# Optimization experiments

Hardware: AMD Instinct MI355X
Metric: run time of the kernel (lower is better)

The kernel has to match this reference:

```python
import jax, jax.numpy as jnp
import numpy as np

N_NODES = 100000
EPS = 1e-5


def gcn_conv(x, edge_index, W, b):
    # PyG GCNConv: add self loops, symmetric normalization, aggregate at target.
    n = x.shape[0]
    xw = x @ W                                  # [N, F_out]
    loop = jnp.arange(n)
    src = jnp.concatenate([edge_index[0], loop])
    dst = jnp.concatenate([edge_index[1], loop])
    deg = jax.ops.segment_sum(jnp.ones_like(dst, dtype=xw.dtype), dst, num_segments=n)
    dinv = jnp.where(deg > 0, jax.lax.rsqrt(deg), 0.0)
    norm = dinv[src] * dinv[dst]                # [E+N]
    out = jax.ops.segment_sum(norm[:, None] * xw[src], dst, num_segments=n)
    return out + b


def batch_norm(x, gamma, beta):
    # training-mode BatchNorm1d over node dim
    m = x.mean(axis=0)
    v = x.var(axis=0)
    return (x - m) * jax.lax.rsqrt(v + EPS) * gamma + beta


def setup_inputs() -> dict:
    key = jax.random.key(0)
    ks = jax.random.split(key, 16)
    dims = [(128, 256), (256, 128), (128, 64)]
    inp = {
        "x": jax.random.normal(ks[0], (N_NODES, 128), dtype=jnp.float32),
        "edge_index": jax.random.randint(ks[1], (2, 1600000), 0, N_NODES),
        "pos_edge_index": jax.random.randint(ks[2], (2, 200000), 0, N_NODES),
        "neg_edge_index": jax.random.randint(ks[3], (2, 200000), 0, N_NODES),
    }
    for i, (fi, fo) in enumerate(dims, start=1):
        inp[f"W{i}"] = jax.random.normal(ks[3 + i], (fi, fo), dtype=jnp.float32) / np.sqrt(fi)
        inp[f"b{i}"] = jnp.zeros((fo,), dtype=jnp.float32)
        inp[f"g{i}"] = jnp.ones((fo,), dtype=jnp.float32)
        inp[f"beta{i}"] = jnp.zeros((fo,), dtype=jnp.float32)
    return inp


def reference(x, edge_index, pos_edge_index, neg_edge_index,
              W1, b1, g1, beta1, W2, b2, g2, beta2, W3, b3, g3, beta3):
    # encode
    h = gcn_conv(x, edge_index, W1, b1)
    h = jax.nn.sigmoid(batch_norm(h, g1, beta1))
    h = gcn_conv(h, edge_index, W2, b2)
    h = jax.nn.sigmoid(batch_norm(h, g2, beta2))
    h = gcn_conv(h, edge_index, W3, b3)
    z = batch_norm(h, g3, beta3)                # [N, 64]
    # decode
    ei = jnp.concatenate([pos_edge_index, neg_edge_index], axis=-1)
    logits = jnp.sum(z[ei[0]] * z[ei[1]], axis=-1)
    return logits
```

## Files before the change

### kernel.cpp

```cpp
#include <hip/hip_runtime.h>
#include <hip/hip_bf16.h>
#include <stddef.h>


#define WAVE 64
#define BSHIFT 9
#define SCHUNK 4096

typedef __attribute__((ext_vector_type(8))) short short8;
typedef __attribute__((ext_vector_type(4))) float f32x4;

__device__ __forceinline__ float bl(uint g) { return __uint_as_float(g << 16); }
__device__ __forceinline__ float bh(uint g) { return __uint_as_float(g & 0xffff0000u); }
__device__ __forceinline__ ushort f2b(float f) {
    uint u = __float_as_uint(f);
    return (ushort)((u + 0x7fffu + ((u >> 16) & 1u)) >> 16);
}
__device__ __forceinline__ uint pack2(float lo, float hi) {
    return (uint)f2b(lo) | ((uint)f2b(hi) << 16);
}

__device__ __forceinline__ void gload16(const ushort* g, ushort* l) {
    __builtin_amdgcn_global_load_lds(
        (const __attribute__((address_space(1))) uint*)g,
        (__attribute__((address_space(3))) uint*)l, 16, 0, 0);
}

__global__ __launch_bounds__(256) void k_bhist(const int* __restrict__ dst, int* __restrict__ gh, int E) {
    __shared__ int lh[256];
    lh[threadIdx.x] = 0; __syncthreads();
    int i = blockIdx.x * 256 + threadIdx.x, stride = gridDim.x * 256;
    for (; i < E; i += stride) atomicAdd(&lh[dst[i] >> BSHIFT], 1);
    __syncthreads();
    int v = lh[threadIdx.x];
    if (v) atomicAdd(&gh[threadIdx.x], v);
}

__global__ void k_bscan(const int* __restrict__ gh, int* __restrict__ boff, int* __restrict__ bcur) {
    __shared__ int ls[256];
    int t = threadIdx.x;
    int v = gh[t];
    ls[t] = v; __syncthreads();
    for (int off = 1; off < 256; off <<= 1) {
        int x = (t >= off) ? ls[t - off] : 0;
        __syncthreads();
        ls[t] += x;
        __syncthreads();
    }
    int excl = ls[t] - v;
    boff[t] = excl; bcur[t] = excl;
    if (t == 255) boff[256] = ls[255];
}

__global__ __launch_bounds__(256) void k_bscatter(const int* __restrict__ src, const int* __restrict__ dst,
                                                  int* __restrict__ gcur, uint* __restrict__ pairs, int E) {
    __shared__ int lh[256];
    int t = threadIdx.x;
    int base = blockIdx.x * SCHUNK;
    lh[t] = 0; __syncthreads();
    int rs[16], rd[16];
    #pragma unroll
    for (int i = 0; i < 16; ++i) {
        int idx = base + i * 256 + t;
        if (idx < E) { rs[i] = src[idx]; rd[i] = dst[idx]; atomicAdd(&lh[rd[i] >> BSHIFT], 1); }
        else rd[i] = -1;
    }
    __syncthreads();
    int cnt_b = lh[t];
    int b0 = cnt_b ? atomicAdd(&gcur[t], cnt_b) : 0;
    lh[t] = b0;
    __syncthreads();
    #pragma unroll
    for (int i = 0; i < 16; ++i) {
        if (rd[i] >= 0) {
            int p = atomicAdd(&lh[rd[i] >> BSHIFT], 1);
            pairs[p] = ((uint)(rd[i] & 511) << 17) | (uint)rs[i];
        }
    }
}

__global__ __launch_bounds__(256) void k_bfine(const uint* __restrict__ pairs, const int* __restrict__ boff,
                                               int* __restrict__ rowptr, int* __restrict__ srcs,
                                               float* __restrict__ dinv, int N, int E) {
    __shared__ int lcnt[512];
    __shared__ int ls[256];
    int b = blockIdx.x, t = threadIdx.x;
    int d0 = b << BSHIFT;
    int e0 = boff[b], e1 = boff[b + 1];
    lcnt[t] = 0; lcnt[t + 256] = 0;
    __syncthreads();
    for (int e = e0 + t; e < e1; e += 256)
        atomicAdd(&lcnt[pairs[e] >> 17], 1);
    __syncthreads();
    int c0 = lcnt[2 * t], c1 = lcnt[2 * t + 1];
    ls[t] = c0 + c1;
    __syncthreads();
    for (int off = 1; off < 256; off <<= 1) {
        int x = (t >= off) ? ls[t - off] : 0;
        __syncthreads();
        ls[t] += x;
        __syncthreads();
    }
    int excl = ls[t] - (c0 + c1);
    int s0 = excl, s1 = excl + c0;
    int d = d0 + 2 * t;
    if (d < N)     { rowptr[d] = e0 + s0;     dinv[d] = rsqrtf((float)(c0 + 1)); }
    if (d + 1 < N) { rowptr[d + 1] = e0 + s1; dinv[d + 1] = rsqrtf((float)(c1 + 1)); }
    if (b == 0 && t == 0) rowptr[N] = E;
    lcnt[2 * t] = s0; lcnt[2 * t + 1] = s1;
    __syncthreads();
    for (int e = e0 + t; e < e1; e += 256) {
        uint p = pairs[e];
        int pos = atomicAdd(&lcnt[p >> 17], 1);
        srcs[e0 + pos] = (int)(p & 0x1FFFFu);
    }
}

__global__ void k_conv(const float* __restrict__ W1, const float* __restrict__ W2,
                       const float* __restrict__ W3, ushort* __restrict__ Wt1,
                       ushort* __restrict__ Wt2, ushort* __restrict__ Wt3,
                       const float* __restrict__ x, const float* __restrict__ dinv,
                       ushort* __restrict__ xs, size_t n4) {
    size_t i = (size_t)blockIdx.x * 256 + threadIdx.x;
    if (i < 73728) {
        const float* W; ushort* Wt; int K, Nn; size_t j;
        if (i < 32768)      { W = W1; Wt = Wt1; K = 128; Nn = 256; j = i; }
        else if (i < 65536) { W = W2; Wt = Wt2; K = 256; Nn = 128; j = i - 32768; }
        else                { W = W3; Wt = Wt3; K = 128; Nn = 64;  j = i - 65536; }
        int k = (int)(j / Nn), n = (int)(j % Nn);
        Wt[(size_t)n * K + k] = f2b(W[(size_t)k * Nn + n]);
        return;
    }
    size_t j = i - 73728;
    if (j >= n4) return;
    float d = dinv[j / 32];
    float4 v = reinterpret_cast<const float4*>(x)[j];
    uint2 o;
    o.x = pack2(d * v.x, d * v.y);
    o.y = pack2(d * v.z, d * v.w);
    reinterpret_cast<uint2*>(xs)[j] = o;
}

template<int F>
__global__ __launch_bounds__(256) void k_agg(const ushort* __restrict__ in, ushort* __restrict__ out,
                                             const int* __restrict__ rowptr, const int* __restrict__ srcs,
                                             const float* __restrict__ dinv, int N) {
    constexpr int L = (F * 2) / 16;
    int wv = threadIdx.x >> 6, lane = threadIdx.x & 63;
    int node = (blockIdx.x * 4 + wv) * (64 / L) + lane / L;
    int sl = lane % L;
    if (node >= N) return;
    const uint4* inq = reinterpret_cast<const uint4*>(in);
    float di = dinv[node];
    float acc[8];
    {
        uint4 v = inq[(size_t)node * L + sl];
        acc[0] = bl(v.x); acc[1] = bh(v.x);
        acc[2] = bl(v.y); acc[3] = bh(v.y);
        acc[4] = bl(v.z); acc[5] = bh(v.z);
        acc[6] = bl(v.w); acc[7] = bh(v.w);
    }
    int e = rowptr[node], e1 = rowptr[node + 1];
    for (; e + 7 < e1; e += 8) {
        int s[8];
        #pragma unroll
        for (int i = 0; i < 8; ++i) s[i] = srcs[e + i];
        uint4 v[8];
        #pragma unroll
        for (int i = 0; i < 8; ++i) v[i] = inq[(size_t)s[i] * L + sl];
        #pragma unroll
        for (int i = 0; i < 8; ++i) {
            acc[0] += bl(v[i].x); acc[1] += bh(v[i].x);
            acc[2] += bl(v[i].y); acc[3] += bh(v[i].y);
            acc[4] += bl(v[i].z); acc[5] += bh(v[i].z);
            acc[6] += bl(v[i].w); acc[7] += bh(v[i].w);
        }
    }
    for (; e + 3 < e1; e += 4) {
        int s[4];
        #pragma unroll
        for (int i = 0; i < 4; ++i) s[i] = srcs[e + i];
        uint4 v[4];
        #pragma unroll
        for (int i = 0; i < 4; ++i) v[i] = inq[(size_t)s[i] * L + sl];
        #pragma unroll
        for (int i = 0; i < 4; ++i) {
            acc[0] += bl(v[i].x); acc[1] += bh(v[i].x);
            acc[2] += bl(v[i].y); acc[3] += bh(v[i].y);
            acc[4] += bl(v[i].z); acc[5] += bh(v[i].z);
            acc[6] += bl(v[i].w); acc[7] += bh(v[i].w);
        }
    }
    for (; e < e1; ++e) {
        uint4 v0 = inq[(size_t)srcs[e] * L + sl];
        acc[0] += bl(v0.x); acc[1] += bh(v0.x);
        acc[2] += bl(v0.y); acc[3] += bh(v0.y);
        acc[4] += bl(v0.z); acc[5] += bh(v0.z);
        acc[6] += bl(v0.w); acc[7] += bh(v0.w);
    }
    uint4 o;
    o.x = pack2(acc[0] * di, acc[1] * di);
    o.y = pack2(acc[2] * di, acc[3] * di);
    o.z = pack2(acc[4] * di, acc[5] * di);
    o.w = pack2(acc[6] * di, acc[7] * di);
    reinterpret_cast<uint4*>(out)[(size_t)node * L + sl] = o;
}

template<int F>
__global__ __launch_bounds__(256) void k_bnstats(const ushort* __restrict__ h, float* __restrict__ gsum,
                                                 float* __restrict__ gsq, int N) {
    constexpr int C = F / 8;
    constexpr int RPW = 64 / C;
    __shared__ float ls[4][16][16];
    int wv = threadIdx.x >> 6, lane = threadIdx.x & 63;
    int fidx = lane % C, rsub = lane / C;
    int row = (blockIdx.x * 4 + wv) * RPW + rsub;
    int rstride = gridDim.x * 4 * RPW;
    const uint4* hq = reinterpret_cast<const uint4*>(h);
    float s[8] = {}, q[8] = {};
    for (int r = row; r < N; r += rstride) {
        uint4 v = hq[(size_t)r * C + fidx];
        float x;
        x = bl(v.x); s[0] += x; q[0] += x * x;
        x = bh(v.x); s[1] += x; q[1] += x * x;
        x = bl(v.y); s[2] += x; q[2] += x * x;
        x = bh(v.y); s[3] += x; q[3] += x * x;
        x = bl(v.z); s[4] += x; q[4] += x * x;
        x = bh(v.z); s[5] += x; q[5] += x * x;
        x = bl(v.w); s[6] += x; q[6] += x * x;
        x = bh(v.w); s[7] += x; q[7] += x * x;
    }
    #pragma unroll
    for (int m = C; m < 64; m <<= 1) {
        #pragma unroll
        for (int j = 0; j < 8; ++j) { s[j] += __shfl_xor(s[j], m); q[j] += __shfl_xor(q[j], m); }
    }
    if (lane < C) {
        #pragma unroll
        for (int j = 0; j < 8; ++j) { ls[wv][lane][j] = s[j]; ls[wv][lane][8 + j] = q[j]; }
    }
    __syncthreads();
    int t = threadIdx.x;
    if (t < F) {
        int ch = t / 8, j = t % 8;
        float S = 0.f, Q = 0.f;
        #pragma unroll
        for (int w = 0; w < 4; ++w) { S += ls[w][ch][j]; Q += ls[w][ch][8 + j]; }
        atomicAdd(&gsum[t], S); atomicAdd(&gsq[t], Q);
    }
}

template<int F>
__global__ __launch_bounds__(256) void k_apply(ushort* __restrict__ h,
                                               const float* __restrict__ bsum, const float* __restrict__ bsq,
                                               const float* __restrict__ bg, const float* __restrict__ bb,
                                               float invN, long NT) {
    constexpr int CPR = F / 8;
    int tid = blockIdx.x * 256 + threadIdx.x;
    int fb = (tid % CPR) * 8;
    float sc[8], sh[8];
    #pragma unroll
    for (int j = 0; j < 8; ++j) {
        float m = bsum[fb + j] * invN;
        float var = bsq[fb + j] * invN - m * m;
        float s = bg[fb + j] * rsqrtf(var + 1e-5f);
        sc[j] = s; sh[j] = bb[fb + j] - m * s;
    }
    uint4* hq = reinterpret_cast<uint4*>(h);
    long stride = (long)gridDim.x * 256;
    for (long i = tid; i < NT; i += stride) {
        uint4 v = hq[i];
        float x[8];
        x[0] = bl(v.x); x[1] = bh(v.x); x[2] = bl(v.y); x[3] = bh(v.y);
        x[4] = bl(v.z); x[5] = bh(v.z); x[6] = bl(v.w); x[7] = bh(v.w);
        #pragma unroll
        for (int j = 0; j < 8; ++j) {
            float y = x[j] * sc[j] + sh[j];
            x[j] = 1.f / (1.f + __expf(-y));
        }
        v.x = pack2(x[0], x[1]); v.y = pack2(x[2], x[3]);
        v.z = pack2(x[4], x[5]); v.w = pack2(x[6], x[7]);
        hq[i] = v;
    }
}

template<int K, int NF, int NPASS, bool STATS, bool PRESCALE>
__global__ __launch_bounds__(256) void k_gemm(const ushort* __restrict__ A, const ushort* __restrict__ Wt,
                                              ushort* __restrict__ C, int M, int Nout,
                                              const float* __restrict__ dinv,
                                              float* __restrict__ gsum, float* __restrict__ gsq) {
    constexpr int S = K / 64;
    constexpr int KS = K / 32;
    __shared__ ushort Alds[2][128 * 64];
    int m0 = blockIdx.x * 128;
    int t = threadIdx.x;
    int w = t >> 6, lane = t & 63;
    int wr = w >> 1, wc = w & 1;
    int rf = lane & 15, kg = lane >> 4;

    auto stage = [&](int buf, int step) {
        #pragma unroll
        for (int i = 0; i < 4; ++i) {
            int cb = (i * 4 + w) * 64;
            int chunk = cb + lane;
            int r = chunk >> 3, cs = chunk & 7;
            int c = cs ^ (r & 7);
            int gr = m0 + r; if (gr >= M) gr = M - 1;
            gload16(A + (size_t)gr * K + step * 64 + c * 8, &Alds[buf][cb * 8]);
        }
    };

    float dreg[4][4];
    if constexpr (PRESCALE) {
        #pragma unroll
        for (int mf = 0; mf < 4; ++mf)
            #pragma unroll
            for (int j = 0; j < 4; ++j) {
                int row = m0 + wr * 64 + mf * 16 + kg * 4 + j;
                dreg[mf][j] = (row < M) ? dinv[row] : 0.f;
            }
    }

    for (int pass = 0; pass < NPASS; ++pass) {
        int n0 = pass * NF * 32;
        const ushort* bp[NF];
        #pragma unroll
        for (int nf = 0; nf < NF; ++nf)
            bp[nf] = Wt + (size_t)(n0 + wc * (NF * 16) + nf * 16 + rf) * K + kg * 8;

        f32x4 acc[4][NF];
        #pragma unroll
        for (int mf = 0; mf < 4; ++mf)
            #pragma unroll
            for (int nf = 0; nf < NF; ++nf)
                acc[mf][nf] = (f32x4){0.f, 0.f, 0.f, 0.f};

        if (pass == 0) {
            stage(0, 0);
            if constexpr (S == 2) stage(1, 1);
            __syncthreads();
        }

        short8 bcur[NF];
        #pragma unroll
        for (int nf = 0; nf < NF; ++nf)
            bcur[nf] = *reinterpret_cast<const short8*>(bp[nf]);

        for (int s = 0; s < S; ++s) {
            if constexpr (S > 2) {
                if (s + 1 < S && pass == 0) stage((s + 1) & 1, s + 1);
            }
            #pragma unroll
            for (int ksl = 0; ksl < 2; ++ksl) {
                int gs = s * 2 + ksl;
                short8 bnxt[NF];
                if (gs + 1 < KS) {
                    #pragma unroll
                    for (int nf = 0; nf < NF; ++nf)
                        bnxt[nf] = *reinterpret_cast<const short8*>(bp[nf] + (gs + 1) * 32);
                }
                short8 a[4];
                #pragma unroll
                for (int mf = 0; mf < 4; ++mf) {
                    int R = wr * 64 + mf * 16 + rf;
                    int idx = R * 8 + ((ksl * 4 + kg) ^ (R & 7));
                    a[mf] = *reinterpret_cast<const short8*>(&Alds[s & 1][idx * 8]);
                }
                #pragma unroll
                for (int mf = 0; mf < 4; ++mf)
                    #pragma unroll
                    for (int nf = 0; nf < NF; ++nf)
                        acc[mf][nf] = __builtin_amdgcn_mfma_f32_16x16x32_bf16(a[mf], bcur[nf], acc[mf][nf], 0, 0, 0);
                if (gs + 1 < KS) {
                    #pragma unroll
                    for (int nf = 0; nf < NF; ++nf) bcur[nf] = bnxt[nf];
                }
            }
            if constexpr (S > 2) __syncthreads();
        }

        #pragma unroll
        for (int mf = 0; mf < 4; ++mf)
            #pragma unroll
            for (int nf = 0; nf < NF; ++nf) {
                int col = n0 + wc * (NF * 16) + nf * 16 + rf;
                #pragma unroll
                for (int j = 0; j < 4; ++j) {
                    int row = m0 + wr * 64 + mf * 16 + kg * 4 + j;
                    float v = acc[mf][nf][j];
                    if constexpr (PRESCALE) v *= dreg[mf][j];
                    if (row < M) C[(size_t)row * Nout + col] = f2b(v);
                }
            }

        if constexpr (STATS) {
            __shared__ float bns[2][NF * 32], bnq[2][NF * 32];
            __syncthreads();
            #pragma unroll
            for (int nf = 0; nf < NF; ++nf) {
                float cs = 0.f, cq = 0.f;
                #pragma unroll
                for (int mf = 0; mf < 4; ++mf)
                    #pragma unroll
                    for (int j = 0; j < 4; ++j) {
                        int row = m0 + wr * 64 + mf * 16 + kg * 4 + j;
                        float v = (row < M) ? acc[mf][nf][j] : 0.f;
                        cs += v; cq += v * v;
                    }
                cs += __shfl_xor(cs, 16); cs += __shfl_xor(cs, 32);
                cq += __shfl_xor(cq, 16); cq += __shfl_xor(cq, 32);
                if (kg == 0) { bns[wr][wc * (NF * 16) + nf * 16 + rf] = cs; bnq[wr][wc * (NF * 16) + nf * 16 + rf] = cq; }
            }
            __syncthreads();
            if (t < NF * 32) {
                atomicAdd(&gsum[n0 + t], bns[0][t] + bns[1][t]);
                atomicAdd(&gsq[n0 + t],  bnq[0][t] + bnq[1][t]);
            }
        }
    }
}

__global__ __launch_bounds__(256) void k_decode(const ushort* __restrict__ h,
                                                const float* __restrict__ bsum, const float* __restrict__ bsq,
                                                const float* __restrict__ bg, const float* __restrict__ bb,
                                                float invN,
                                                const int* __restrict__ pos, const int* __restrict__ neg,
                                                int Pp, int Pn, float* __restrict__ out) {
    __shared__ float scl[64], shl[64];
    int t = threadIdx.x;
    if (t < 64) {
        float m = bsum[t] * invN;
        float var = bsq[t] * invN - m * m;
        float sc = bg[t] * rsqrtf(var + 1e-5f);
        scl[t] = sc; shl[t] = bb[t] - m * sc;
    }
    __syncthreads();
    int gid = blockIdx.x * 16 + (t >> 4);
    int l = t & 15;
    int P = Pp + Pn;
    if (gid >= P) return;
    int a, b;
    if (gid < Pp) { a = pos[gid]; b = pos[Pp + gid]; }
    else          { int e = gid - Pp; a = neg[e]; b = neg[Pn + e]; }
    const uint2* hu = reinterpret_cast<const uint2*>(h);
    uint2 ua = hu[(size_t)a * 16 + l];
    uint2 ub = hu[(size_t)b * 16 + l];
    int f = l * 4;
    float s0 = scl[f], s1 = scl[f + 1], s2 = scl[f + 2], s3 = scl[f + 3];
    float t0 = shl[f], t1 = shl[f + 1], t2 = shl[f + 2], t3 = shl[f + 3];
    float a0 = bl(ua.x) * s0 + t0, a1 = bh(ua.x) * s1 + t1, a2 = bl(ua.y) * s2 + t2, a3 = bh(ua.y) * s3 + t3;
    float b0 = bl(ub.x) * s0 + t0, b1 = bh(ub.x) * s1 + t1, b2 = bl(ub.y) * s2 + t2, b3 = bh(ub.y) * s3 + t3;
    float d = a0 * b0 + a1 * b1 + a2 * b2 + a3 * b3;
    d += __shfl_xor(d, 1);
    d += __shfl_xor(d, 2);
    d += __shfl_xor(d, 4);
    d += __shfl_xor(d, 8);
    if (l == 0) out[gid] = d;
}

extern "C" void kernel_launch(void* const* d_in, const int* in_sizes, int n_in,
                              void* d_out, int out_size, void* d_ws, size_t ws_size,
                              hipStream_t stream) {
    const float* x   = (const float*)d_in[0];
    const int*   ei  = (const int*)d_in[1];
    const int*   pe  = (const int*)d_in[2];
    const int*   ne  = (const int*)d_in[3];
    const float* W1  = (const float*)d_in[4];
    const float* g1  = (const float*)d_in[6];
    const float* be1 = (const float*)d_in[7];
    const float* W2  = (const float*)d_in[8];
    const float* g2  = (const float*)d_in[10];
    const float* be2 = (const float*)d_in[11];
    const float* W3  = (const float*)d_in[12];
    const float* g3  = (const float*)d_in[14];
    const float* be3 = (const float*)d_in[15];
    float* out = (float*)d_out;

    const int N  = in_sizes[0] / 128;
    const int E  = in_sizes[1] / 2;
    const int Pp = in_sizes[2] / 2;
    const int Pn = in_sizes[3] / 2;
    const float invN = 1.0f / (float)N;

    char* ws = (char*)d_ws;
    auto carve = [&](size_t bytes) -> char* {
        char* p = ws;
        ws += (bytes + 255) & ~(size_t)255;
        return p;
    };
    char*  zz     = carve(256 * 4 + 896 * 4);
    int*   gh     = (int*)zz;
    float* sums1  = (float*)(zz + 1024);
    float* sq1    = sums1 + 256;
    float* sums2  = sq1 + 256;
    float* sq2    = sums2 + 128;
    float* sums3  = sq2 + 128;
    float* sq3    = sums3 + 64;
    size_t zz_bytes = 1024 + 896 * 4;

    int*    boff   = (int*)carve(257 * 4);
    int*    bcur   = (int*)carve(256 * 4);
    int*    rowptr = (int*)carve((size_t)(N + 1) * 4);
    float*  dinv   = (float*)carve((size_t)N * 4);
    int*    srcs   = (int*)carve((size_t)E * 4);
    uint*   pairs  = (uint*)carve((size_t)E * 4);
    ushort* Wt1    = (ushort*)carve(128 * 256 * 2);
    ushort* Wt2    = (ushort*)carve(256 * 128 * 2);
    ushort* Wt3    = (ushort*)carve(128 * 64 * 2);
    ushort* b1     = (ushort*)carve((size_t)N * 128 * 2);
    ushort* b2     = (ushort*)carve((size_t)N * 128 * 2);
    ushort* b3     = (ushort*)carve((size_t)N * 256 * 2);

    const int* e_src = ei;
    const int* e_dst = ei + E;
    const int NBUCK = (N + (1 << BSHIFT) - 1) >> BSHIFT;

    hipMemsetAsync(zz, 0, zz_bytes, stream);

    k_bhist<<<2048, 256, 0, stream>>>(e_dst, gh, E);
    k_bscan<<<1, 256, 0, stream>>>(gh, boff, bcur);
    k_bscatter<<<(E + SCHUNK - 1) / SCHUNK, 256, 0, stream>>>(e_src, e_dst, bcur, pairs, E);
    k_bfine<<<NBUCK, 256, 0, stream>>>(pairs, boff, rowptr, srcs, dinv, N, E);

    {
        size_t n4 = (size_t)N * 128 / 4;
        int blocks = (int)((73728 + n4 + 255) / 256);
        k_conv<<<blocks, 256, 0, stream>>>(W1, W2, W3, Wt1, Wt2, Wt3, x, dinv, b1, n4);
    }

    const int mblk = (N + 127) / 128;
    const int agg128 = (N + 15) / 16;
    const int agg64  = (N + 31) / 32;

    k_agg<128><<<agg128, 256, 0, stream>>>(b1, b2, rowptr, srcs, dinv, N);
    k_gemm<128, 4, 2, true, false><<<mblk, 256, 0, stream>>>(b2, Wt1, b3, N, 256, nullptr, sums1, sq1);
    k_apply<256><<<2048, 256, 0, stream>>>(b3, sums1, sq1, g1, be1, invN, (long)N * 32);

    k_gemm<256, 4, 1, false, true><<<mblk, 256, 0, stream>>>(b3, Wt2, b1, N, 128, dinv, nullptr, nullptr);
    k_agg<128><<<agg128, 256, 0, stream>>>(b1, b2, rowptr, srcs, dinv, N);
    k_bnstats<128><<<512, 256, 0, stream>>>(b2, sums2, sq2, N);
    k_apply<128><<<2048, 256, 0, stream>>>(b2, sums2, sq2, g2, be2, invN, (long)N * 16);

    k_gemm<128, 2, 1, false, true><<<mblk, 256, 0, stream>>>(b2, Wt3, b1, N, 64, dinv, nullptr, nullptr);
    k_agg<64><<<agg64, 256, 0, stream>>>(b1, b2, rowptr, srcs, dinv, N);
    k_bnstats<64><<<512, 256, 0, stream>>>(b2, sums3, sq3, N);

    k_decode<<<(Pp + Pn + 15) / 16, 256, 0, stream>>>(b2, sums3, sq3, g3, be3, invN,
                                                      pe, ne, Pp, Pn, out);
}
```

Measured before the change: 536.6 us.

## Fuse BN-apply+sigmoid into GEMM A-staging and BN stats into aggregation

Removes the standalone k_apply and k_bnstats kernels. The BatchNorm scale/shift and sigmoid are now applied while the next GEMM loads A tiles into LDS, with synchronous loads replacing the async global_load_lds path. Per-feature sum and sum-of-squares are reduced inside the aggregation kernel through wave shuffles and atomics. This saves several full passes over the activations and four launches. In exchange the GEMM staging is no longer asynchronous and each block recomputes the BN coefficients and evaluates exp.

Measured after the change: 658.0 us. +22.6%, slower.

```diff
diff --git a/kernel.cpp b/kernel.cpp
--- a/kernel.cpp
+++ b/kernel.cpp
@@ -141,154 +141,107 @@
     reinterpret_cast<uint2*>(xs)[j] = o;
 }
 
-template<int F>
+template<int F, bool STATS>
 __global__ __launch_bounds__(256) void k_agg(const ushort* __restrict__ in, ushort* __restrict__ out,
                                              const int* __restrict__ rowptr, const int* __restrict__ srcs,
-                                             const float* __restrict__ dinv, int N) {
+                                             const float* __restrict__ dinv, int N,
+                                             float* __restrict__ gsum, float* __restrict__ gsq) {
     constexpr int L = (F * 2) / 16;
     int wv = threadIdx.x >> 6, lane = threadIdx.x & 63;
     int node = (blockIdx.x * 4 + wv) * (64 / L) + lane / L;
     int sl = lane % L;
-    if (node >= N) return;
+    bool act = node < N;
     const uint4* inq = reinterpret_cast<const uint4*>(in);
-    float di = dinv[node];
-    float acc[8];
-    {
-        uint4 v = inq[(size_t)node * L + sl];
-        acc[0] = bl(v.x); acc[1] = bh(v.x);
-        acc[2] = bl(v.y); acc[3] = bh(v.y);
-        acc[4] = bl(v.z); acc[5] = bh(v.z);
-        acc[6] = bl(v.w); acc[7] = bh(v.w);
-    }
-    int e = rowptr[node], e1 = rowptr[node + 1];
-    for (; e + 7 < e1; e += 8) {
-        int s[8];
-        #pragma unroll
-        for (int i = 0; i < 8; ++i) s[i] = srcs[e + i];
-        uint4 v[8];
-        #pragma unroll
-        for (int i = 0; i < 8; ++i) v[i] = inq[(size_t)s[i] * L + sl];
-        #pragma unroll
-        for (int i = 0; i < 8; ++i) {
-            acc[0] += bl(v[i].x); acc[1] += bh(v[i].x);
-            acc[2] += bl(v[i].y); acc[3] += bh(v[i].y);
-            acc[4] += bl(v[i].z); acc[5] += bh(v[i].z);
-            acc[6] += bl(v[i].w); acc[7] += bh(v[i].w);
-        }
-    }
-    for (; e + 3 < e1; e += 4) {
-        int s[4];
-        #pragma unroll
-        for (int i = 0; i < 4; ++i) s[i] = srcs[e + i];
-        uint4 v[4];
-        #pragma unroll
-        for (int i = 0; i < 4; ++i) v[i] = inq[(size_t)s[i] * L + sl];
-        #pragma unroll
-        for (int i = 0; i < 4; ++i) {
-            acc[0] += bl(v[i].x); acc[1] += bh(v[i].x);
-            acc[2] += bl(v[i].y); acc[3] += bh(v[i].y);
-            acc[4] += bl(v[i].z); acc[5] += bh(v[i].z);
-            acc[6] += bl(v[i].w); acc[7] += bh(v[i].w);
-        }
-    }
-    for (; e < e1; ++e) {
-        uint4 v0 = inq[(size_t)srcs[e] * L + sl];
-        acc[0] += bl(v0.x); acc[1] += bh(v0.x);
-        acc[2] += bl(v0.y); acc[3] += bh(v0.y);
-        acc[4] += bl(v0.z); acc[5] += bh(v0.z);
-        acc[6] += bl(v0.w); acc[7] += bh(v0.w);
-    }
-    uint4 o;
-    o.x = pack2(acc[0] * di, acc[1] * di);
-    o.y = pack2(acc[2] * di, acc[3] * di);
-    o.z = pack2(acc[4] * di, acc[5] * di);
-    o.w = pack2(acc[6] * di, acc[7] * di);
-    reinterpret_cast<uint4*>(out)[(size_t)node * L + sl] = o;
-}
-
-template<int F>
-__global__ __launch_bounds__(256) void k_bnstats(const ushort* __restrict__ h, float* __restrict__ gsum,
-                                                 float* __restrict__ gsq, int N) {
-    constexpr int C = F / 8;
-    constexpr int RPW = 64 / C;
-    __shared__ float ls[4][16][16];
-    int wv = threadIdx.x >> 6, lane = threadIdx.x & 63;
-    int fidx = lane % C, rsub = lane / C;
-    int row = (blockIdx.x * 4 + wv) * RPW + rsub;
-    int rstride = gridDim.x * 4 * RPW;
-    const uint4* hq = reinterpret_cast<const uint4*>(h);
-    float s[8] = {}, q[8] = {};
-    for (int r = row; r < N; r += rstride) {
-        uint4 v = hq[(size_t)r * C + fidx];
-        float x;
-        x = bl(v.x); s[0] += x; q[0] += x * x;
-        x = bh(v.x); s[1] += x; q[1] += x * x;
-        x = bl(v.y); s[2] += x; q[2] += x * x;
-        x = bh(v.y); s[3] += x; q[3] += x * x;
-        x = bl(v.z); s[4] += x; q[4] += x * x;
-        x = bh(v.z); s[5] += x; q[5] += x * x;
-        x = bl(v.w); s[6] += x; q[6] += x * x;
-        x = bh(v.w); s[7] += x; q[7] += x * x;
-    }
-    #pragma unroll
-    for (int m = C; m < 64; m <<= 1) {
-        #pragma unroll
-        for (int j = 0; j < 8; ++j) { s[j] += __shfl_xor(s[j], m); q[j] += __shfl_xor(q[j], m); }
-    }
-    if (lane < C) {
-        #pragma unroll
-        for (int j = 0; j < 8; ++j) { ls[wv][lane][j] = s[j]; ls[wv][lane][8 + j] = q[j]; }
-    }
-    __syncthreads();
-    int t = threadIdx.x;
-    if (t < F) {
-        int ch = t / 8, j = t % 8;
-        float S = 0.f, Q = 0.f;
-        #pragma unroll
-        for (int w = 0; w < 4; ++w) { S += ls[w][ch][j]; Q += ls[w][ch][8 + j]; }
-        atomicAdd(&gsum[t], S); atomicAdd(&gsq[t], Q);
-    }
-}
-
-template<int F>
-__global__ __launch_bounds__(256) void k_apply(ushort* __restrict__ h,
-                                               const float* __restrict__ bsum, const float* __restrict__ bsq,
-                                               const float* __restrict__ bg, const float* __restrict__ bb,
-                                               float invN, long NT) {
-    constexpr int CPR = F / 8;
-    int tid = blockIdx.x * 256 + threadIdx.x;
-    int fb = (tid % CPR) * 8;
-    float sc[8], sh[8];
-    #pragma unroll
-    for (int j = 0; j < 8; ++j) {
-        float m = bsum[fb + j] * invN;
-        float var = bsq[fb + j] * invN - m * m;
-        float s = bg[fb + j] * rsqrtf(var + 1e-5f);
-        sc[j] = s; sh[j] = bb[fb + j] - m * s;
-    }
-    uint4* hq = reinterpret_cast<uint4*>(h);
-    long stride = (long)gridDim.x * 256;
-    for (long i = tid; i < NT; i += stride) {
-        uint4 v = hq[i];
-        float x[8];
-        x[0] = bl(v.x); x[1] = bh(v.x); x[2] = bl(v.y); x[3] = bh(v.y);
-        x[4] = bl(v.z); x[5] = bh(v.z); x[6] = bl(v.w); x[7] = bh(v.w);
-        #pragma unroll
-        for (int j = 0; j < 8; ++j) {
-            float y = x[j] * sc[j] + sh[j];
-            x[j] = 1.f / (1.f + __expf(-y));
-        }
-        v.x = pack2(x[0], x[1]); v.y = pack2(x[2], x[3]);
-        v.z = pack2(x[4], x[5]); v.w = pack2(x[6], x[7]);
-        hq[i] = v;
-    }
-}
-
-template<int K, int NF, int NPASS, bool STATS, bool PRESCALE>
+    float o[8] = {0.f, 0.f, 0.f, 0.f, 0.f, 0.f, 0.f, 0.f};
+    if (act) {
+        float di = dinv[node];
+        float acc[8];
+        {
+            uint4 v = inq[(size_t)node * L + sl];
+            acc[0] = bl(v.x); acc[1] = bh(v.x);
+            acc[2] = bl(v.y); acc[3] = bh(v.y);
+            acc[4] = bl(v.z); acc[5] = bh(v.z);
+            acc[6] = bl(v.w); acc[7] = bh(v.w);
+        }
+        int e = rowptr[node], e1 = rowptr[node + 1];
+        for (; e + 7 < e1; e += 8) {
+            int s[8];
+            #pragma unroll
+            for (int i = 0; i < 8; ++i) s[i] = srcs[e + i];
+            uint4 v[8];
+            #pragma unroll
+            for (int i = 0; i < 8; ++i) v[i] = inq[(size_t)s[i] * L + sl];
+            #pragma unroll
+            for (int i = 0; i < 8; ++i) {
+                acc[0] += bl(v[i].x); acc[1] += bh(v[i].x);
+                acc[2] += bl(v[i].y); acc[3] += bh(v[i].y);
+                acc[4] += bl(v[i].z); acc[5] += bh(v[i].z);
+                acc[6] += bl(v[i].w); acc[7] += bh(v[i].w);
+            }
+        }
+        for (; e + 3 < e1; e += 4) {
+            int s[4];
+            #pragma unroll
+            for (int i = 0; i < 4; ++i) s[i] = srcs[e + i];
+            uint4 v[4];
+            #pragma unroll
+            for (int i = 0; i < 4; ++i) v[i] = inq[(size_t)s[i] * L + sl];
+            #pragma unroll
+            for (int i = 0; i < 4; ++i) {
+                acc[0] += bl(v[i].x); acc[1] += bh(v[i].x);
+                acc[2] += bl(v[i].y); acc[3] += bh(v[i].y);
+                acc[4] += bl(v[i].z); acc[5] += bh(v[i].z);
+                acc[6] += bl(v[i].w); acc[7] += bh(v[i].w);
+            }
+        }
+        for (; e < e1; ++e) {
+            uint4 v0 = inq[(size_t)srcs[e] * L + sl];
+            acc[0] += bl(v0.x); acc[1] += bh(v0.x);
+            acc[2] += bl(v0.y); acc[3] += bh(v0.y);
+            acc[4] += bl(v0.z); acc[5] += bh(v0.z);
+            acc[6] += bl(v0.w); acc[7] += bh(v0.w);
+        }
+        #pragma unroll
+        for (int j = 0; j < 8; ++j) o[j] = acc[j] * di;
+        uint4 ov;
+        ov.x = pack2(o[0], o[1]); ov.y = pack2(o[2], o[3]);
+        ov.z = pack2(o[4], o[5]); ov.w = pack2(o[6], o[7]);
+        reinterpret_cast<uint4*>(out)[(size_t)node * L + sl] = ov;
+    }
+    if constexpr (STATS) {
+        __shared__ float lsum[4][L][8], lsq[4][L][8];
+        float s[8], q[8];
+        #pragma unroll
+        for (int j = 0; j < 8; ++j) { s[j] = o[j]; q[j] = o[j] * o[j]; }
+        #pragma unroll
+        for (int m = L; m < 64; m <<= 1) {
+            #pragma unroll
+            for (int j = 0; j < 8; ++j) { s[j] += __shfl_xor(s[j], m); q[j] += __shfl_xor(q[j], m); }
+        }
+        if (lane < L) {
+            #pragma unroll
+            for (int j = 0; j < 8; ++j) { lsum[wv][lane][j] = s[j]; lsq[wv][lane][j] = q[j]; }
+        }
+        __syncthreads();
+        int t = threadIdx.x;
+        if (t < F) {
+            int ch = t / 8, j = t % 8;
+            float S = 0.f, Q = 0.f;
+            #pragma unroll
+            for (int w = 0; w < 4; ++w) { S += lsum[w][ch][j]; Q += lsq[w][ch][j]; }
+            atomicAdd(&gsum[t], S); atomicAdd(&gsq[t], Q);
+        }
+    }
+}
+
+template<int K, int NF, int NPASS, bool STATS, bool PRESCALE, bool APPLY>
 __global__ __launch_bounds__(256) void k_gemm(const ushort* __restrict__ A, const ushort* __restrict__ Wt,
                                               ushort* __restrict__ C, int M, int Nout,
                                               const float* __restrict__ dinv,
-                                              float* __restrict__ gsum, float* __restrict__ gsq) {
+                                              float* __restrict__ gsum, float* __restrict__ gsq,
+                                              const float* __restrict__ bsum, const float* __restrict__ bsq,
+                                              const float* __restrict__ bg, const float* __restrict__ bb,
+                                              float invN) {
     constexpr int S = K / 64;
     constexpr int KS = K / 32;
     __shared__ ushort Alds[2][128 * 64];
@@ -310,6 +263,40 @@
         }
     };
 
+    int cg_ = (t & 7) ^ ((t >> 3) & 7);
+    auto stageA = [&](int buf, int s) {
+        float sc[8], sh[8];
+        int fb = s * 64 + cg_ * 8;
+        #pragma unroll
+        for (int j = 0; j < 8; ++j) {
+            float m = bsum[fb + j] * invN;
+            float var = bsq[fb + j] * invN - m * m;
+            float sv = bg[fb + j] * rsqrtf(var + 1e-5f);
+            sc[j] = sv; sh[j] = bb[fb + j] - m * sv;
+        }
+        #pragma unroll
+        for (int i = 0; i < 4; ++i) {
+            int r = (t >> 3) + i * 32;
+            int gr = m0 + r; if (gr >= M) gr = M - 1;
+            uint4 v = *reinterpret_cast<const uint4*>(A + (size_t)gr * K + s * 64 + cg_ * 8);
+            uint u[4] = {v.x, v.y, v.z, v.w};
+            #pragma unroll
+            for (int j = 0; j < 4; ++j) {
+                float x0 = bl(u[j]) * sc[2 * j] + sh[2 * j];
+                float x1 = bh(u[j]) * sc[2 * j + 1] + sh[2 * j + 1];
+                x0 = 1.f / (1.f + __expf(-x0));
+                x1 = 1.f / (1.f + __expf(-x1));
+                u[j] = pack2(x0, x1);
+            }
+            v.x = u[0]; v.y = u[1]; v.z = u[2]; v.w = u[3];
+            *reinterpret_cast<uint4*>(&Alds[buf][(size_t)(r * 8 + (t & 7)) * 8]) = v;
+        }
+    };
+
+    auto do_stage = [&](int buf, int step) {
+        if constexpr (APPLY) stageA(buf, step); else stage(buf, step);
+    };
+
     float dreg[4][4];
     if constexpr (PRESCALE) {
         #pragma unroll
@@ -336,8 +323,8 @@
                 acc[mf][nf] = (f32x4){0.f, 0.f, 0.f, 0.f};
 
         if (pass == 0) {
-            stage(0, 0);
-            if constexpr (S == 2) stage(1, 1);
+            do_stage(0, 0);
+            if constexpr (S == 2) do_stage(1, 1);
             __syncthreads();
         }
 
@@ -348,7 +335,7 @@
 
         for (int s = 0; s < S; ++s) {
             if constexpr (S > 2) {
-                if (s + 1 < S && pass == 0) stage((s + 1) & 1, s + 1);
+                if (s + 1 < S && pass == 0) do_stage((s + 1) & 1, s + 1);
             }
             #pragma unroll
             for (int ksl = 0; ksl < 2; ++ksl) {
@@ -532,18 +519,17 @@
     const int agg128 = (N + 15) / 16;
     const int agg64  = (N + 31) / 32;
 
-    k_agg<128><<<agg128, 256, 0, stream>>>(b1, b2, rowptr, srcs, dinv, N);
-    k_gemm<128, 4, 2, true, false><<<mblk, 256, 0, stream>>>(b2, Wt1, b3, N, 256, nullptr, sums1, sq1);
-    k_apply<256><<<2048, 256, 0, stream>>>(b3, sums1, sq1, g1, be1, invN, (long)N * 32);
-
-    k_gemm<256, 4, 1, false, true><<<mblk, 256, 0, stream>>>(b3, Wt2, b1, N, 128, dinv, nullptr, nullptr);
-    k_agg<128><<<agg128, 256, 0, stream>>>(b1, b2, rowptr, srcs, dinv, N);
-    k_bnstats<128><<<512, 256, 0, stream>>>(b2, sums2, sq2, N);
-    k_apply<128><<<2048, 256, 0, stream>>>(b2, sums2, sq2, g2, be2, invN, (long)N * 16);
-
-    k_gemm<128, 2, 1, false, true><<<mblk, 256, 0, stream>>>(b2, Wt3, b1, N, 64, dinv, nullptr, nullptr);
-    k_agg<64><<<agg64, 256, 0, stream>>>(b1, b2, rowptr, srcs, dinv, N);
-    k_bnstats<64><<<512, 256, 0, stream>>>(b2, sums3, sq3, N);
+    k_agg<128, false><<<agg128, 256, 0, stream>>>(b1, b2, rowptr, srcs, dinv, N, nullptr, nullptr);
+    k_gemm<128, 4, 2, true, false, false><<<mblk, 256, 0, stream>>>(
+        b2, Wt1, b3, N, 256, nullptr, sums1, sq1, nullptr, nullptr, nullptr, nullptr, invN);
+
+    k_gemm<256, 4, 1, false, true, true><<<mblk, 256, 0, stream>>>(
+        b3, Wt2, b1, N, 128, dinv, nullptr, nullptr, sums1, sq1, g1, be1, invN);
+    k_agg<128, true><<<agg128, 256, 0, stream>>>(b1, b2, rowptr, srcs, dinv, N, sums2, sq2);
+
+    k_gemm<128, 2, 1, false, true, true><<<mblk, 256, 0, stream>>>(
+        b2, Wt3, b1, N, 64, dinv, nullptr, nullptr, sums2, sq2, g2, be2, invN);
+    k_agg<64, true><<<agg64, 256, 0, stream>>>(b1, b2, rowptr, srcs, dinv, N, sums3, sq3);
 
     k_decode<<<(Pp + Pn + 15) / 16, 256, 0, stream>>>(b2, sums3, sq3, g3, be3, invN,
                                                       pe, ne, Pp, Pn, out);
```

## Stage whole A tile in LDS, add 64-row GEMM tile, fuse weight conversion into histogram

Applied to the files above, without the earlier changes.

The GEMM now loads the full K-wide A tile into LDS in one pass instead of double-buffering 64-column slices, which removes the per-step barriers. A BM template parameter is added so the K=256 GEMM can use 64-row tiles with four column-wave groups, doubling the block count for that layer. The weight transpose/convert work moves out of the x-conversion kernel into the histogram kernel as extra blocks, so it overlaps with edge counting. The single-shot LDS tile uses 32KB per block for both K=128 and K=256, which may limit occupancy, and the load no longer overlaps with MFMA work.

Result: no change. 540.0 us (+0.6%).

```diff
diff --git a/kernel.cpp b/kernel.cpp
--- a/kernel.cpp
+++ b/kernel.cpp
@@ -6,6 +6,8 @@
 #define WAVE 64
 #define BSHIFT 9
 #define SCHUNK 4096
+#define HB 2048
+#define WB 288
 
 typedef __attribute__((ext_vector_type(8))) short short8;
 typedef __attribute__((ext_vector_type(4))) float f32x4;
@@ -26,14 +28,28 @@
         (__attribute__((address_space(3))) uint*)l, 16, 0, 0);
 }
 
-__global__ __launch_bounds__(256) void k_bhist(const int* __restrict__ dst, int* __restrict__ gh, int E) {
-    __shared__ int lh[256];
-    lh[threadIdx.x] = 0; __syncthreads();
-    int i = blockIdx.x * 256 + threadIdx.x, stride = gridDim.x * 256;
-    for (; i < E; i += stride) atomicAdd(&lh[dst[i] >> BSHIFT], 1);
-    __syncthreads();
-    int v = lh[threadIdx.x];
-    if (v) atomicAdd(&gh[threadIdx.x], v);
+__global__ __launch_bounds__(256) void k_pre(const int* __restrict__ dst, int* __restrict__ gh, int E,
+                                             const float* __restrict__ W1, const float* __restrict__ W2,
+                                             const float* __restrict__ W3, ushort* __restrict__ Wt1,
+                                             ushort* __restrict__ Wt2, ushort* __restrict__ Wt3) {
+    int b = blockIdx.x, t = threadIdx.x;
+    if (b < HB) {
+        __shared__ int lh[256];
+        lh[t] = 0; __syncthreads();
+        for (int i = b * 256 + t; i < E; i += HB * 256) atomicAdd(&lh[dst[i] >> BSHIFT], 1);
+        __syncthreads();
+        int v = lh[t];
+        if (v) atomicAdd(&gh[t], v);
+    } else {
+        int i = (b - HB) * 256 + t;
+        const float* W; ushort* Wt; int K, Nn, j;
+        if (i < 32768)      { W = W1; Wt = Wt1; K = 128; Nn = 256; j = i; }
+        else if (i < 65536) { W = W2; Wt = Wt2; K = 256; Nn = 128; j = i - 32768; }
+        else if (i < 73728) { W = W3; Wt = Wt3; K = 128; Nn = 64;  j = i - 65536; }
+        else return;
+        int k = j / Nn, n = j % Nn;
+        Wt[(size_t)n * K + k] = f2b(W[(size_t)k * Nn + n]);
+    }
 }
 
 __global__ void k_bscan(const int* __restrict__ gh, int* __restrict__ boff, int* __restrict__ bcur) {
@@ -116,22 +132,9 @@
     }
 }
 
-__global__ void k_conv(const float* __restrict__ W1, const float* __restrict__ W2,
-                       const float* __restrict__ W3, ushort* __restrict__ Wt1,
-                       ushort* __restrict__ Wt2, ushort* __restrict__ Wt3,
-                       const float* __restrict__ x, const float* __restrict__ dinv,
-                       ushort* __restrict__ xs, size_t n4) {
-    size_t i = (size_t)blockIdx.x * 256 + threadIdx.x;
-    if (i < 73728) {
-        const float* W; ushort* Wt; int K, Nn; size_t j;
-        if (i < 32768)      { W = W1; Wt = Wt1; K = 128; Nn = 256; j = i; }
-        else if (i < 65536) { W = W2; Wt = Wt2; K = 256; Nn = 128; j = i - 32768; }
-        else                { W = W3; Wt = Wt3; K = 128; Nn = 64;  j = i - 65536; }
-        int k = (int)(j / Nn), n = (int)(j % Nn);
-        Wt[(size_t)n * K + k] = f2b(W[(size_t)k * Nn + n]);
-        return;
-    }
-    size_t j = i - 73728;
+__global__ void k_convx(const float* __restrict__ x, const float* __restrict__ dinv,
+                        ushort* __restrict__ xs, size_t n4) {
+    size_t j = (size_t)blockIdx.x * 256 + threadIdx.x;
     if (j >= n4) return;
     float d = dinv[j / 32];
     float4 v = reinterpret_cast<const float4*>(x)[j];
@@ -284,31 +287,31 @@
     }
 }
 
-template<int K, int NF, int NPASS, bool STATS, bool PRESCALE>
+template<int BM, int K, int NF, int NPASS, bool STATS, bool PRESCALE>
 __global__ __launch_bounds__(256) void k_gemm(const ushort* __restrict__ A, const ushort* __restrict__ Wt,
                                               ushort* __restrict__ C, int M, int Nout,
                                               const float* __restrict__ dinv,
                                               float* __restrict__ gsum, float* __restrict__ gsq) {
-    constexpr int S = K / 64;
+    constexpr int CH = K / 8;
     constexpr int KS = K / 32;
-    __shared__ ushort Alds[2][128 * 64];
-    int m0 = blockIdx.x * 128;
+    constexpr int WN = (BM == 128) ? 2 : 4;
+    __shared__ uint4 Alds[BM * CH];
+    int m0 = blockIdx.x * BM;
     int t = threadIdx.x;
     int w = t >> 6, lane = t & 63;
-    int wr = w >> 1, wc = w & 1;
+    int wr = w / WN, wc = w % WN;
     int rf = lane & 15, kg = lane >> 4;
 
-    auto stage = [&](int buf, int step) {
-        #pragma unroll
-        for (int i = 0; i < 4; ++i) {
-            int cb = (i * 4 + w) * 64;
-            int chunk = cb + lane;
-            int r = chunk >> 3, cs = chunk & 7;
-            int c = cs ^ (r & 7);
-            int gr = m0 + r; if (gr >= M) gr = M - 1;
-            gload16(A + (size_t)gr * K + step * 64 + c * 8, &Alds[buf][cb * 8]);
-        }
-    };
+    #pragma unroll
+    for (int i = 0; i < 8; ++i) {
+        int cb = (i * 4 + w) * 64;
+        int d = cb + lane;
+        int r = d / CH, cs = d % CH;
+        int c = cs ^ (r & 7);
+        int gr = m0 + r; if (gr >= M) gr = M - 1;
+        gload16(A + (size_t)gr * K + c * 8, (ushort*)&Alds[cb]);
+    }
+    __syncthreads();
 
     float dreg[4][4];
     if constexpr (PRESCALE) {
@@ -322,7 +325,7 @@
     }
 
     for (int pass = 0; pass < NPASS; ++pass) {
-        int n0 = pass * NF * 32;
+        int n0 = pass * WN * NF * 16;
         const ushort* bp[NF];
         #pragma unroll
         for (int nf = 0; nf < NF; ++nf)
@@ -335,48 +338,34 @@
             for (int nf = 0; nf < NF; ++nf)
                 acc[mf][nf] = (f32x4){0.f, 0.f, 0.f, 0.f};
 
-        if (pass == 0) {
-            stage(0, 0);
-            if constexpr (S == 2) stage(1, 1);
-            __syncthreads();
-        }
-
         short8 bcur[NF];
         #pragma unroll
         for (int nf = 0; nf < NF; ++nf)
             bcur[nf] = *reinterpret_cast<const short8*>(bp[nf]);
 
-        for (int s = 0; s < S; ++s) {
-            if constexpr (S > 2) {
-                if (s + 1 < S && pass == 0) stage((s + 1) & 1, s + 1);
-            }
+        for (int gs = 0; gs < KS; ++gs) {
+            short8 bnxt[NF];
+            if (gs + 1 < KS) {
+                #pragma unroll
+                for (int nf = 0; nf < NF; ++nf)
+                    bnxt[nf] = *reinterpret_cast<const short8*>(bp[nf] + (gs + 1) * 32);
+            }
+            short8 a[4];
             #pragma unroll
-            for (int ksl = 0; ksl < 2; ++ksl) {
-                int gs = s * 2 + ksl;
-                short8 bnxt[NF];
-                if (gs + 1 < KS) {
-                    #pragma unroll
-                    for (int nf = 0; nf < NF; ++nf)
-                        bnxt[nf] = *reinterpret_cast<const short8*>(bp[nf] + (gs + 1) * 32);
-                }
-                short8 a[4];
+            for (int mf = 0; mf < 4; ++mf) {
+                int R = wr * 64 + mf * 16 + rf;
+                int q = gs * 4 + kg;
+                a[mf] = *reinterpret_cast<const short8*>(&Alds[R * CH + (q ^ (R & 7))]);
+            }
+            #pragma unroll
+            for (int mf = 0; mf < 4; ++mf)
                 #pragma unroll
-                for (int mf = 0; mf < 4; ++mf) {
-                    int R = wr * 64 + mf * 16 + rf;
-                    int idx = R * 8 + ((ksl * 4 + kg) ^ (R & 7));
-                    a[mf] = *reinterpret_cast<const short8*>(&Alds[s & 1][idx * 8]);
-                }
+                for (int nf = 0; nf < NF; ++nf)
+                    acc[mf][nf] = __builtin_amdgcn_mfma_f32_16x16x32_bf16(a[mf], bcur[nf], acc[mf][nf], 0, 0, 0);
+            if (gs + 1 < KS) {
                 #pragma unroll
-                for (int mf = 0; mf < 4; ++mf)
-                    #pragma unroll
-                    for (int nf = 0; nf < NF; ++nf)
-                        acc[mf][nf] = __builtin_amdgcn_mfma_f32_16x16x32_bf16(a[mf], bcur[nf], acc[mf][nf], 0, 0, 0);
-                if (gs + 1 < KS) {
-                    #pragma unroll
-                    for (int nf = 0; nf < NF; ++nf) bcur[nf] = bnxt[nf];
-                }
-            }
-            if constexpr (S > 2) __syncthreads();
+                for (int nf = 0; nf < NF; ++nf) bcur[nf] = bnxt[nf];
+            }
         }
 
         #pragma unroll
@@ -394,7 +383,7 @@
             }
 
         if constexpr (STATS) {
-            __shared__ float bns[2][NF * 32], bnq[2][NF * 32];
+            __shared__ float bns[4 / WN][WN * NF * 16], bnq[4 / WN][WN * NF * 16];
             __syncthreads();
             #pragma unroll
             for (int nf = 0; nf < NF; ++nf) {
@@ -412,9 +401,12 @@
                 if (kg == 0) { bns[wr][wc * (NF * 16) + nf * 16 + rf] = cs; bnq[wr][wc * (NF * 16) + nf * 16 + rf] = cq; }
             }
             __syncthreads();
-            if (t < NF * 32) {
-                atomicAdd(&gsum[n0 + t], bns[0][t] + bns[1][t]);
-                atomicAdd(&gsq[n0 + t],  bnq[0][t] + bnq[1][t]);
+            if (t < WN * NF * 16) {
+                float S = 0.f, Q = 0.f;
+                #pragma unroll
+                for (int r2 = 0; r2 < 4 / WN; ++r2) { S += bns[r2][t]; Q += bnq[r2][t]; }
+                atomicAdd(&gsum[n0 + t], S);
+                atomicAdd(&gsq[n0 + t],  Q);
             }
         }
     }
@@ -517,31 +509,34 @@
 
     hipMemsetAsync(zz, 0, zz_bytes, stream);
 
-    k_bhist<<<2048, 256, 0, stream>>>(e_dst, gh, E);
+    k_pre<<<HB + WB, 256, 0, stream>>>(e_dst, gh, E, W1, W2, W3, Wt1, Wt2, Wt3);
     k_bscan<<<1, 256, 0, stream>>>(gh, boff, bcur);
     k_bscatter<<<(E + SCHUNK - 1) / SCHUNK, 256, 0, stream>>>(e_src, e_dst, bcur, pairs, E);
     k_bfine<<<NBUCK, 256, 0, stream>>>(pairs, boff, rowptr, srcs, dinv, N, E);
 
     {
         size_t n4 = (size_t)N * 128 / 4;
-        int blocks = (int)((73728 + n4 + 255) / 256);
-        k_conv<<<blocks, 256, 0, stream>>>(W1, W2, W3, Wt1, Wt2, Wt3, x, dinv, b1, n4);
-    }
-
-    const int mblk = (N + 127) / 128;
-    const int agg128 = (N + 15) / 16;
-    const int agg64  = (N + 31) / 32;
+        k_convx<<<(int)((n4 + 255) / 256), 256, 0, stream>>>(x, dinv, b1, n4);
+    }
+
+    const int mblk128 = (N + 127) / 128;
+    const int mblk64  = (N + 63) / 64;
+    const int agg128  = (N + 15) / 16;
+    const int agg64   = (N + 31) / 32;
 
     k_agg<128><<<agg128, 256, 0, stream>>>(b1, b2, rowptr, srcs, dinv, N);
-    k_gemm<128, 4, 2, true, false><<<mblk, 256, 0, stream>>>(b2, Wt1, b3, N, 256, nullptr, sums1, sq1);
+    k_gemm<128, 128, 4, 2, true, false><<<mblk128, 256, 0, stream>>>(
+        b2, Wt1, b3, N, 256, nullptr, sums1, sq1);
     k_apply<256><<<2048, 256, 0, stream>>>(b3, sums1, sq1, g1, be1, invN, (long)N * 32);
 
-    k_gemm<256, 4, 1, false, true><<<mblk, 256, 0, stream>>>(b3, Wt2, b1, N, 128, dinv, nullptr, nullptr);
+    k_gemm<64, 256, 2, 1, false, true><<<mblk64, 256, 0, stream>>>(
+        b3, Wt2, b1, N, 128, dinv, nullptr, nullptr);
     k_agg<128><<<agg128, 256, 0, stream>>>(b1, b2, rowptr, srcs, dinv, N);
     k_bnstats<128><<<512, 256, 0, stream>>>(b2, sums2, sq2, N);
     k_apply<128><<<2048, 256, 0, stream>>>(b2, sums2, sq2, g2, be2, invN, (long)N * 16);
 
-    k_gemm<128, 2, 1, false, true><<<mblk, 256, 0, stream>>>(b2, Wt3, b1, N, 64, dinv, nullptr, nullptr);
+    k_gemm<128, 128, 2, 1, false, true><<<mblk128, 256, 0, stream>>>(
+        b2, Wt3, b1, N, 64, dinv, nullptr, nullptr);
     k_agg<64><<<agg64, 256, 0, stream>>>(b1, b2, rowptr, srcs, dinv, N);
     k_bnstats<64><<<512, 256, 0, stream>>>(b2, sums3, sq3, N);
 
```
